# Optimization experiments

Measured on AMD Instinct MI355X. Metric: run time of the kernel, lower is better.

## Reference

```python
import jax, jax.numpy as jnp
import numpy as np

NUM_GROUPS = 8
INPUT_DIM = 1024
OUTPUT_DIM = 1024
TOKENS_PER_GROUP = 8192  # rows per group after reshape


def setup_inputs() -> dict:
    key = jax.random.key(0)
    kx, kw = jax.random.split(key)
    # x: [N*G, D_in] as fed to the torch module (it reshapes internally)
    x = jax.random.normal(kx, (TOKENS_PER_GROUP * NUM_GROUPS, INPUT_DIM), dtype=jnp.float32)
    # Stacked per-group Linear weights, torch layout [D_out, D_in] per group.
    # Xavier-normal gain=1: std = sqrt(2 / (fan_in + fan_out))
    std = np.sqrt(2.0 / (INPUT_DIM + OUTPUT_DIM)).astype(np.float32)
    W = jax.random.normal(kw, (NUM_GROUPS, OUTPUT_DIM, INPUT_DIM), dtype=jnp.float32) * std
    return {"x": x, "W": W}


def reference(x, W):
    # x: [N*G, D_in] -> [N, G, D_in]
    n = x.shape[0] // NUM_GROUPS
    xg = x.reshape(n, NUM_GROUPS, INPUT_DIM)
    # per-group linear: out[n,g,k] = sum_d xg[n,g,d] * W[g,k,d]
    out = jnp.einsum("ngd,gkd->ngk", xg, W)
    return out.reshape(-1, OUTPUT_DIM)
```

## Files before the change

kernel.cpp:

```cpp
#include <hip/hip_runtime.h>
#include <hip/hip_bf16.h>


namespace {

constexpr int NG   = 8;
constexpr int DIN  = 1024;
constexpr int DOUT = 1024;
constexpr int BM   = 256;
constexpr int BN   = 256;
constexpr int BK   = 64;
constexpr int NKT  = DIN / BK;
constexpr int ROWB = BK * 2;
constexpr int LDS_TILE  = BM * ROWB;
constexpr int LDS_BYTES = 4 * LDS_TILE;

typedef __attribute__((ext_vector_type(8))) short bf16x8;
typedef __attribute__((ext_vector_type(4))) float f32x4;

__device__ __forceinline__ uint2 pack_bf16x4(f32x4 v) {
  union { __hip_bfloat162 h2[2]; uint2 u; } p;
  p.h2[0] = __float22bfloat162_rn(make_float2(v.x, v.y));
  p.h2[1] = __float22bfloat162_rn(make_float2(v.z, v.w));
  return p.u;
}

#define FENCE() asm volatile("" ::: "memory")
#define BAR()   do { FENCE(); __builtin_amdgcn_s_barrier(); FENCE(); } while (0)
#define LGKM0() asm volatile("s_waitcnt lgkmcnt(0)" ::: "memory")

#define QPHASE(Q, PRE, POST)                                                   \
  do {                                                                         \
    bf16x8 a0k0 = *(const bf16x8*)(cA + aRow0 + (2*(Q))   * 2048 + colx0);     \
    bf16x8 a0k1 = *(const bf16x8*)(cA + aRow0 + (2*(Q))   * 2048 + colx1);     \
    bf16x8 a1k0 = *(const bf16x8*)(cA + aRow0 + (2*(Q)+1) * 2048 + colx0);     \
    bf16x8 a1k1 = *(const bf16x8*)(cA + aRow0 + (2*(Q)+1) * 2048 + colx1);     \
    PRE                                                                        \
    BAR();                                                                     \
    LGKM0();                                                                   \
    __builtin_amdgcn_sched_barrier(0);                                         \
    __builtin_amdgcn_s_setprio(1);                                             \
    _Pragma("unroll")                                                          \
    for (int n = 0; n < 4; ++n) {                                              \
      acc[2*(Q)][n]   = __builtin_amdgcn_mfma_f32_16x16x32_bf16(               \
          a0k0, bfr[n][0], acc[2*(Q)][n],   0, 0, 0);                          \
      acc[2*(Q)][n]   = __builtin_amdgcn_mfma_f32_16x16x32_bf16(               \
          a0k1, bfr[n][1], acc[2*(Q)][n],   0, 0, 0);                          \
      acc[2*(Q)+1][n] = __builtin_amdgcn_mfma_f32_16x16x32_bf16(               \
          a1k0, bfr[n][0], acc[2*(Q)+1][n], 0, 0, 0);                          \
      acc[2*(Q)+1][n] = __builtin_amdgcn_mfma_f32_16x16x32_bf16(               \
          a1k1, bfr[n][1], acc[2*(Q)+1][n], 0, 0, 0);                          \
    }                                                                          \
    __builtin_amdgcn_s_setprio(0);                                             \
    POST                                                                       \
    BAR();                                                                     \
  } while (0)

__global__ __launch_bounds__(512, 2)
void grouped_gemm_8p(const float* __restrict__ X,
                     const float* __restrict__ W,
                     float* __restrict__ O) {
  extern __shared__ char smem[];
  char* const smA = smem;
  char* const smB = smem + 2 * LDS_TILE;

  const int bid = (int)blockIdx.x;
  const int swz = (bid & 7) * 128 + (bid >> 3);
  const int jt = swz & 3;
  const int it = (swz >> 2) & 31;
  const int g  = swz >> 7;

  const int n0 = it * BM;
  const int c0 = jt * BN;

  const int tid  = (int)threadIdx.x;
  const int lane = tid & 63;
  const int wid  = tid >> 6;
  const int wr   = wid >> 2;
  const int wc   = wid & 3;

  const int s_lane = tid & 15;
  const int s_row  = tid >> 4;

  const float* Ag = X + ((size_t)(n0 + s_row) * NG + g) * DIN + s_lane * 4;
  const float* Bg = W + (size_t)g * DOUT * DIN + (size_t)(c0 + s_row) * DIN
                      + s_lane * 4;
  constexpr size_t ASTR = (size_t)32 * NG * DIN;
  constexpr size_t BSTR = (size_t)32 * DIN;

  const int wb0 = s_row * ROWB + ((s_lane * 8) ^ ((s_row & 7) << 4));

  const int fr = lane & 15;
  const int fq = lane >> 4;
  const int swzm  = (fr & 7) << 4;
  const int colx0 = (fq * 16) ^ swzm;
  const int colx1 = (64 + fq * 16) ^ swzm;
  const int aRow0 = (wr * 128 + fr) * ROWB;
  const int bRow0 = (wc * 64  + fr) * ROWB;

  f32x4 aS[8], bS[8];
  f32x4 acc[8][4];
#pragma unroll
  for (int m = 0; m < 8; ++m)
#pragma unroll
    for (int n = 0; n < 4; ++n) acc[m][n] = (f32x4){0.f, 0.f, 0.f, 0.f};

#pragma unroll
  for (int p = 0; p < 8; ++p) {
    aS[p] = *(const f32x4*)(Ag + p * ASTR);
    bS[p] = *(const f32x4*)(Bg + p * BSTR);
  }
#pragma unroll
  for (int p = 0; p < 8; ++p) {
    *(uint2*)(smA + wb0 + p * 4096) = pack_bf16x4(aS[p]);
    *(uint2*)(smB + wb0 + p * 4096) = pack_bf16x4(bS[p]);
  }
  LGKM0();
  BAR();

#pragma unroll 2
  for (int t = 0; t < NKT; ++t) {
    char* const cA = smA + (t & 1) * LDS_TILE;
    char* const cB = smB + (t & 1) * LDS_TILE;
    char* const nA = smA + ((t & 1) ^ 1) * LDS_TILE;
    char* const nB = smB + ((t & 1) ^ 1) * LDS_TILE;
    const bool stage = (t + 1) < NKT;

    bf16x8 bfr[4][2];
#pragma unroll
    for (int n = 0; n < 4; ++n) {
      bfr[n][0] = *(const bf16x8*)(cB + bRow0 + n * 2048 + colx0);
      bfr[n][1] = *(const bf16x8*)(cB + bRow0 + n * 2048 + colx1);
    }

    QPHASE(0,
      { if (stage) {
          const float* An = Ag + (size_t)(t + 1) * BK;
          for (int p = 0; p < 8; ++p) aS[p] = *(const f32x4*)(An + p * ASTR);
        } },
      { });

    QPHASE(1, { },
      { if (stage) {
          for (int p = 0; p < 8; ++p)
            *(uint2*)(nA + wb0 + p * 4096) = pack_bf16x4(aS[p]);
        } });

    QPHASE(2,
      { if (stage) {
          const float* Bn = Bg + (size_t)(t + 1) * BK;
          for (int p = 0; p < 8; ++p) bS[p] = *(const f32x4*)(Bn + p * BSTR);
        } },
      { });

    QPHASE(3, { },
      { if (stage) {
          for (int p = 0; p < 8; ++p)
            *(uint2*)(nB + wb0 + p * 4096) = pack_bf16x4(bS[p]);
        }
        LGKM0(); });
  }

#pragma unroll
  for (int m = 0; m < 8; ++m) {
#pragma unroll
    for (int r = 0; r < 4; ++r) {
      const int row = wr * 128 + m * 16 + fq * 4 + r;
      float* orow = O + ((size_t)(n0 + row) * NG + g) * DOUT + c0 + wc * 64;
#pragma unroll
      for (int n = 0; n < 4; ++n) {
        orow[n * 16 + fr] = acc[m][n][r];
      }
    }
  }
}

}

extern "C" void kernel_launch(void* const* d_in, const int* in_sizes, int n_in,
                              void* d_out, int out_size, void* d_ws, size_t ws_size,
                              hipStream_t stream) {
  (void)n_in; (void)d_ws; (void)ws_size; (void)out_size;
  const float* X = (const float*)d_in[0];
  const float* W = (const float*)d_in[1];
  float* O = (float*)d_out;

  const int tokens_total = in_sizes[0] / DIN;
  const int ntok_per_g   = tokens_total / NG;
  const int grid = NG * (ntok_per_g / BM) * (DOUT / BN);

  (void)hipFuncSetAttribute((const void*)grouped_gemm_8p,
                            hipFuncAttributeMaxDynamicSharedMemorySize,
                            LDS_BYTES);

  grouped_gemm_8p<<<dim3(grid), dim3(512), LDS_BYTES, stream>>>(X, W, O);
}
```

Baseline: 266.4 us.

## Reorder MFMA phases by k-half and issue both global prefetches earlier

Each phase now covers four A row-fragments at one k-half instead of two row-fragments at both k-halves. This halves the B fragment registers held at once, since the second-half B fragments are loaded mid-iteration. Both the A and B global prefetches for the next tile now issue in the first two phases, giving the B loads more time to land before they are written to LDS. The staging loops are also explicitly unrolled. The aim is to cut register pressure and hide global latency better, at the cost of an extra LDS read sequence for B inside the loop.

```diff
diff --git a/kernel.cpp b/kernel.cpp
--- a/kernel.cpp
+++ b/kernel.cpp
@@ -28,13 +28,15 @@
 #define FENCE() asm volatile("" ::: "memory")
 #define BAR()   do { FENCE(); __builtin_amdgcn_s_barrier(); FENCE(); } while (0)
 #define LGKM0() asm volatile("s_waitcnt lgkmcnt(0)" ::: "memory")
-
-#define QPHASE(Q, PRE, POST)                                                   \
+#define MFMA_(a, b, c) __builtin_amdgcn_mfma_f32_16x16x32_bf16((a), (b), (c), 0, 0, 0)
+
+#define QPHASE(KS, MH, PRE, POST)                                              \
   do {                                                                         \
-    bf16x8 a0k0 = *(const bf16x8*)(cA + aRow0 + (2*(Q))   * 2048 + colx0);     \
-    bf16x8 a0k1 = *(const bf16x8*)(cA + aRow0 + (2*(Q))   * 2048 + colx1);     \
-    bf16x8 a1k0 = *(const bf16x8*)(cA + aRow0 + (2*(Q)+1) * 2048 + colx0);     \
-    bf16x8 a1k1 = *(const bf16x8*)(cA + aRow0 + (2*(Q)+1) * 2048 + colx1);     \
+    const int cx_ = (KS) ? colx1 : colx0;                                      \
+    bf16x8 af0 = *(const bf16x8*)(cA + aRow0 + ((MH)*4+0)*2048 + cx_);         \
+    bf16x8 af1 = *(const bf16x8*)(cA + aRow0 + ((MH)*4+1)*2048 + cx_);         \
+    bf16x8 af2 = *(const bf16x8*)(cA + aRow0 + ((MH)*4+2)*2048 + cx_);         \
+    bf16x8 af3 = *(const bf16x8*)(cA + aRow0 + ((MH)*4+3)*2048 + cx_);         \
     PRE                                                                        \
     BAR();                                                                     \
     LGKM0();                                                                   \
@@ -42,14 +44,10 @@
     __builtin_amdgcn_s_setprio(1);                                             \
     _Pragma("unroll")                                                          \
     for (int n = 0; n < 4; ++n) {                                              \
-      acc[2*(Q)][n]   = __builtin_amdgcn_mfma_f32_16x16x32_bf16(               \
-          a0k0, bfr[n][0], acc[2*(Q)][n],   0, 0, 0);                          \
-      acc[2*(Q)][n]   = __builtin_amdgcn_mfma_f32_16x16x32_bf16(               \
-          a0k1, bfr[n][1], acc[2*(Q)][n],   0, 0, 0);                          \
-      acc[2*(Q)+1][n] = __builtin_amdgcn_mfma_f32_16x16x32_bf16(               \
-          a1k0, bfr[n][0], acc[2*(Q)+1][n], 0, 0, 0);                          \
-      acc[2*(Q)+1][n] = __builtin_amdgcn_mfma_f32_16x16x32_bf16(               \
-          a1k1, bfr[n][1], acc[2*(Q)+1][n], 0, 0, 0);                          \
+      acc[(MH)*4+0][n] = MFMA_(af0, bfr[n], acc[(MH)*4+0][n]);                 \
+      acc[(MH)*4+1][n] = MFMA_(af1, bfr[n], acc[(MH)*4+1][n]);                 \
+      acc[(MH)*4+2][n] = MFMA_(af2, bfr[n], acc[(MH)*4+2][n]);                 \
+      acc[(MH)*4+3][n] = MFMA_(af3, bfr[n], acc[(MH)*4+3][n]);                 \
     }                                                                          \
     __builtin_amdgcn_s_setprio(0);                                             \
     POST                                                                       \
@@ -126,35 +124,41 @@
     char* const nB = smB + ((t & 1) ^ 1) * LDS_TILE;
     const bool stage = (t + 1) < NKT;
 
-    bf16x8 bfr[4][2];
-#pragma unroll
-    for (int n = 0; n < 4; ++n) {
-      bfr[n][0] = *(const bf16x8*)(cB + bRow0 + n * 2048 + colx0);
-      bfr[n][1] = *(const bf16x8*)(cB + bRow0 + n * 2048 + colx1);
-    }
-
-    QPHASE(0,
+    bf16x8 bfr[4];
+#pragma unroll
+    for (int n = 0; n < 4; ++n)
+      bfr[n] = *(const bf16x8*)(cB + bRow0 + n * 2048 + colx0);
+
+    QPHASE(0, 0,
       { if (stage) {
           const float* An = Ag + (size_t)(t + 1) * BK;
+          _Pragma("unroll")
           for (int p = 0; p < 8; ++p) aS[p] = *(const f32x4*)(An + p * ASTR);
         } },
       { });
 
-    QPHASE(1, { },
-      { if (stage) {
+    QPHASE(0, 1,
+      { if (stage) {
+          const float* Bn = Bg + (size_t)(t + 1) * BK;
+          _Pragma("unroll")
+          for (int p = 0; p < 8; ++p) bS[p] = *(const f32x4*)(Bn + p * BSTR);
+        } },
+      { });
+
+    QPHASE(1, 0,
+      { _Pragma("unroll")
+        for (int n = 0; n < 4; ++n)
+          bfr[n] = *(const bf16x8*)(cB + bRow0 + n * 2048 + colx1);
+      },
+      { if (stage) {
+          _Pragma("unroll")
           for (int p = 0; p < 8; ++p)
             *(uint2*)(nA + wb0 + p * 4096) = pack_bf16x4(aS[p]);
         } });
 
-    QPHASE(2,
-      { if (stage) {
-          const float* Bn = Bg + (size_t)(t + 1) * BK;
-          for (int p = 0; p < 8; ++p) bS[p] = *(const f32x4*)(Bn + p * BSTR);
-        } },
-      { });
-
-    QPHASE(3, { },
-      { if (stage) {
+    QPHASE(1, 1, { },
+      { if (stage) {
+          _Pragma("unroll")
           for (int p = 0; p < 8; ++p)
             *(uint2*)(nB + wb0 + p * 4096) = pack_bf16x4(bS[p]);
         }
```

Result: slower. 302.0 us (+13.4%).
